# Performance work log

Measured on AMD Instinct MI355X. Metric: run time of the kernel, lower is better.

Reference implementation:

```python
import jax, jax.numpy as jnp
import numpy as np

N_POINTS = 65536
N0 = 65536
N_NEIGH = 32
K = 15
IN_F = 64
OUT_F = 128
RADIUS = 0.1
KP_EXTENT = 1.2 * RADIUS / 5.0  # config.KP_extent * radius / density_parameter
BN_EPS = 1e-6
NEG_SLOPE = 0.1


def setup_inputs() -> dict:
    key = jax.random.key(0)
    ks = jax.random.split(key, 8)
    cloud_scale = 0.05  # neighbor offsets ~ KP_EXTENT so influences are nonzero
    query_points = jax.random.uniform(ks[0], (N_POINTS, 3), jnp.float32) * cloud_scale
    support_points = jax.random.uniform(ks[1], (N0, 3), jnp.float32) * cloud_scale
    neighbors_indices = jax.random.randint(ks[2], (N_POINTS, N_NEIGH), 0, N0, jnp.int32)
    features = jax.random.normal(ks[3], (N0, IN_F), jnp.float32)
    # fixed kernel point dispositions, scaled to the kernel extent
    kernel_points = jax.random.normal(ks[4], (K, 3), jnp.float32) * (KP_EXTENT / 1.5)
    W = jax.random.normal(ks[5], (K, IN_F, OUT_F), jnp.float32) * np.sqrt(2.0 / OUT_F)
    gamma = jnp.ones((OUT_F,), jnp.float32)
    beta = jnp.zeros((OUT_F,), jnp.float32)
    return {
        "query_points": query_points,
        "support_points": support_points,
        "neighbors_indices": neighbors_indices,
        "features": features,
        "kernel_points": kernel_points,
        "W": W,
        "gamma": gamma,
        "beta": beta,
    }


def reference(query_points, support_points, neighbors_indices, features,
              kernel_points, W, gamma, beta):
    # --- KPConv: gather neighbors, kernel-point linear influence, sum aggregation ---
    # shadow point far away with zero features (handles out-of-range indices in original)
    sp = jnp.concatenate([support_points,
                          jnp.full((1, 3), 1e6, support_points.dtype)], axis=0)
    feat = jnp.concatenate([features,
                            jnp.zeros((1, features.shape[1]), features.dtype)], axis=0)
    neighbors = sp[neighbors_indices]                      # [n, m, 3]
    diffs = neighbors - query_points[:, None, :]           # [n, m, 3]
    # squared distances to each kernel point: [n, m, K]
    sq = jnp.sum((diffs[:, :, None, :] - kernel_points[None, None, :, :]) ** 2, axis=-1)
    # linear influence, 'sum' aggregation mode
    all_w = jnp.maximum(0.0, 1.0 - jnp.sqrt(sq) / KP_EXTENT)  # [n, m, K]
    all_w = jnp.transpose(all_w, (0, 2, 1))                   # [n, K, m]
    neighb_x = feat[neighbors_indices]                        # [n, m, in]
    weighted = jnp.einsum('nkm,nmi->nki', all_w, neighb_x)    # [n, K, in]
    x = jnp.einsum('nki,kio->no', weighted, W)                # [n, out]
    # --- BatchNorm1d (training-mode batch stats) + LeakyReLU(0.1) ---
    mean = jnp.mean(x, axis=0)
    var = jnp.var(x, axis=0)
    x = (x - mean) * jax.lax.rsqrt(var + BN_EPS) * gamma + beta
    return jnp.where(x >= 0, x, NEG_SLOPE * x)
```

## Files before the change

### kernel.cpp

```cpp
#include <hip/hip_runtime.h>

#define NPTS  65536
#define NNEI  32
#define NKP   15
#define INF   64
#define OUTF  128
#define PPB   32
#define NW    8
#define KT_N  32
#define NSETS 64
#define INV_KPE 41.666666666666664f
#define BN_EPS 1e-6f
#define NEG_SLOPE 0.1f

typedef __attribute__((ext_vector_type(8))) short  bf16x8;
typedef __attribute__((ext_vector_type(4))) float  f32x4;

__device__ unsigned short g_Wp[KT_N * 8 * 64 * 8];
__device__ unsigned short g_featb[NPTS * INF];
__device__ float g_part[NSETS][2 * OUTF];
__device__ float g_scale[OUTF], g_shift[OUTF];

__device__ __forceinline__ unsigned short f2b(float f) {
    union { float f; unsigned int i; } v; v.f = f;
    unsigned int x = v.i;
    return (unsigned short)((x + 0x7fffu + ((x >> 16) & 1u)) >> 16);
}
__device__ __forceinline__ unsigned int pk2(float a, float b) {
    return (unsigned int)f2b(a) | ((unsigned int)f2b(b) << 16);
}
__device__ __forceinline__ bf16x8 mk8(unsigned int a, unsigned int b,
                                      unsigned int c, unsigned int d) {
    unsigned int t[4] = {a, b, c, d};
    bf16x8 r; __builtin_memcpy(&r, t, 16); return r;
}

__global__ __launch_bounds__(256) void pack_inputs(const float* __restrict__ W,
                                                   const float* __restrict__ feat) {
    const int b = blockIdx.x, t = threadIdx.x;
    if (b < NSETS) g_part[b][t] = 0.0f;
    if (b < 512) {
        int id = b * 256 + t;
        int j  = id & 7;
        int ln = (id >> 3) & 63;
        int nt = (id >> 9) & 7;
        int kt = id >> 12;
        int i  = kt * 32 + ((ln >> 4) * 8) + j;
        int kp = i & 15;
        int ch = i >> 4;
        int o  = nt * 16 + (ln & 15);
        g_Wp[id] = (kp < NKP) ? f2b(W[(kp * 64 + ch) * 128 + o]) : (unsigned short)0;
    } else {
        int id = (b - 512) * 256 + t;
        const float4 v = ((const float4*)feat)[id];
        uint2 r; r.x = pk2(v.x, v.y); r.y = pk2(v.z, v.w);
        ((uint2*)g_featb)[id] = r;
    }
}

__global__ __launch_bounds__(512, 4) void kpconv_fused(
        const float* __restrict__ qp,
        const float* __restrict__ sp,
        const int*   __restrict__ nbr,
        const float* __restrict__ kp,
        float*       __restrict__ out)
{
    __shared__ __align__(16) unsigned short wlds[128 * PPB * 8];
    __shared__ float dbuf[NW][128][3];
    __shared__ int   ibuf[NW][128];

    const int tid  = threadIdx.x;
    const int lane = tid & 63;
    const int wv   = tid >> 6;
    const int q    = lane >> 4;
    const int c16  = lane & 15;
    const int gp0  = blockIdx.x * PPB + wv * 4;

#pragma unroll
    for (int rep = 0; rep < 2; ++rep) {
        const int pt  = rep * 2 + (lane >> 5);
        const int m   = lane & 31;
        const int gpt = gp0 + pt;
        const int idx = nbr[gpt * NNEI + m];
        ibuf[wv][pt * 32 + m] = idx;
        dbuf[wv][pt * 32 + m][0] = sp[idx * 3 + 0] - qp[gpt * 3 + 0];
        dbuf[wv][pt * 32 + m][1] = sp[idx * 3 + 1] - qp[gpt * 3 + 1];
        dbuf[wv][pt * 32 + m][2] = sp[idx * 3 + 2] - qp[gpt * 3 + 2];
    }
    float kx, ky, kz;
    if (c16 < NKP) { kx = kp[c16 * 3]; ky = kp[c16 * 3 + 1]; kz = kp[c16 * 3 + 2]; }
    else           { kx = ky = kz = 1.0e6f; }

    uint2 dcur[8], dnxt[8];
#pragma unroll
    for (int j = 0; j < 8; ++j) {
        const int idx = ibuf[wv][q * 8 + j];
        dcur[j] = *(const uint2*)&g_featb[idx * INF + c16 * 4];
    }

#pragma unroll
    for (int pt = 0; pt < 4; ++pt) {
        const int pl = wv * 4 + pt;

        if (pt < 3) {
#pragma unroll
            for (int j = 0; j < 8; ++j) {
                const int idx = ibuf[wv][(pt + 1) * 32 + q * 8 + j];
                dnxt[j] = *(const uint2*)&g_featb[idx * INF + c16 * 4];
            }
        }

        float w8[8];
#pragma unroll
        for (int j = 0; j < 8; ++j) {
            const int m = pt * 32 + q * 8 + j;
            const float ex = dbuf[wv][m][0] - kx;
            const float ey = dbuf[wv][m][1] - ky;
            const float ez = dbuf[wv][m][2] - kz;
            const float s  = ex * ex + ey * ey + ez * ez;
            const float w  = 1.0f - __builtin_amdgcn_sqrtf(s) * INV_KPE;
            w8[j] = (w > 0.0f) ? w : 0.0f;
        }
        const bf16x8 af = mk8(pk2(w8[0], w8[1]), pk2(w8[2], w8[3]),
                              pk2(w8[4], w8[5]), pk2(w8[6], w8[7]));

        f32x4 acc[4] = {{0.f,0.f,0.f,0.f},{0.f,0.f,0.f,0.f},
                        {0.f,0.f,0.f,0.f},{0.f,0.f,0.f,0.f}};
#pragma unroll
        for (int nt = 0; nt < 4; ++nt) {
            unsigned int dw[4];
#pragma unroll
            for (int p = 0; p < 4; ++p) {
                const unsigned int lo = (nt < 2) ? dcur[2 * p].x     : dcur[2 * p].y;
                const unsigned int hi = (nt < 2) ? dcur[2 * p + 1].x : dcur[2 * p + 1].y;
                dw[p] = (nt & 1) ? ((lo >> 16) | (hi & 0xffff0000u))
                                 : ((lo & 0xffffu) | (hi << 16));
            }
            acc[nt] = __builtin_amdgcn_mfma_f32_16x16x32_bf16(
                af, mk8(dw[0], dw[1], dw[2], dw[3]), acc[nt], 0, 0, 0);
        }

#pragma unroll
        for (int nt = 0; nt < 4; ++nt) {
            uint2 pv;
            pv.x = pk2(acc[nt][0], acc[nt][1]);
            pv.y = pk2(acc[nt][2], acc[nt][3]);
            const int ibase = (c16 * 4 + nt) * 16 + q * 4;
            const int g   = ibase >> 3;
            const int off = ibase & 7;
            const int plx = pl ^ ((g >> 3) & 7);
            *(uint2*)&wlds[(g * PPB + plx) * 8 + off] = pv;
        }

#pragma unroll
        for (int j = 0; j < 8; ++j) dcur[j] = dnxt[j];
    }
    __syncthreads();

    const int nt = wv;
    f32x4 a0 = {0.f,0.f,0.f,0.f}, a1 = {0.f,0.f,0.f,0.f};

    for (int kt = 0; kt < KT_N; ++kt) {
        const int g   = kt * 4 + q;
        const int h   = (g >> 3) & 7;
        const int plx0 = c16 ^ h;
        const int plx1 = (c16 + 16) ^ h;
        const bf16x8 fa0 = *(const bf16x8*)&wlds[(g * PPB + plx0) * 8];
        const bf16x8 fa1 = *(const bf16x8*)&wlds[(g * PPB + plx1) * 8];
        const bf16x8 fb  = *(const bf16x8*)&g_Wp[((kt * 8 + nt) * 64 + lane) * 8];
        a0 = __builtin_amdgcn_mfma_f32_16x16x32_bf16(fa0, fb, a0, 0, 0, 0);
        a1 = __builtin_amdgcn_mfma_f32_16x16x32_bf16(fa1, fb, a1, 0, 0, 0);
    }

    const int rb = blockIdx.x * PPB + q * 4;
    const int c0 = nt * 16 + c16;
    float s = 0.f, qq = 0.f;
#pragma unroll
    for (int r = 0; r < 4; ++r) {
        const float v0 = a0[r], v1 = a1[r];
        out[(rb + r) * OUTF + c0]        = v0;
        out[(rb + 16 + r) * OUTF + c0]   = v1;
        s += v0 + v1; qq += v0 * v0 + v1 * v1;
    }
    s  += __shfl_xor(s, 16);  s  += __shfl_xor(s, 32);
    qq += __shfl_xor(qq, 16); qq += __shfl_xor(qq, 32);
    const int set = blockIdx.x & (NSETS - 1);
    if (lane < 16) {
        atomicAdd(&g_part[set][nt * 16 + lane],        s);
        atomicAdd(&g_part[set][OUTF + nt * 16 + lane], qq);
    }
}

__global__ void bn_scaleshift(const float* __restrict__ gamma,
                              const float* __restrict__ beta) {
    const int o = threadIdx.x;
    float s = 0.f, qq = 0.f;
    for (int i = 0; i < NSETS; ++i) { s += g_part[i][o]; qq += g_part[i][OUTF + o]; }
    const float inv_n = 1.0f / (float)NPTS;
    const float mean  = s * inv_n;
    const float var   = qq * inv_n - mean * mean;
    const float sc    = gamma[o] * rsqrtf(var + BN_EPS);
    g_scale[o] = sc;
    g_shift[o] = beta[o] - mean * sc;
}

__global__ __launch_bounds__(256) void bn_norm(float* __restrict__ x) {
    const int id   = blockIdx.x * 256 + threadIdx.x;
    const int base = id * 4;
    const int o0   = base & 127;
    float4 v = *(const float4*)&x[base];
    const float4 sc = *(const float4*)&g_scale[o0];
    const float4 sf = *(const float4*)&g_shift[o0];
    float y0 = v.x * sc.x + sf.x;
    float y1 = v.y * sc.y + sf.y;
    float y2 = v.z * sc.z + sf.z;
    float y3 = v.w * sc.w + sf.w;
    y0 = (y0 >= 0.f) ? y0 : NEG_SLOPE * y0;
    y1 = (y1 >= 0.f) ? y1 : NEG_SLOPE * y1;
    y2 = (y2 >= 0.f) ? y2 : NEG_SLOPE * y2;
    y3 = (y3 >= 0.f) ? y3 : NEG_SLOPE * y3;
    float4 res = {y0, y1, y2, y3};
    *(float4*)&x[base] = res;
}

extern "C" void kernel_launch(void* const* d_in, const int* in_sizes, int n_in,
                              void* d_out, int out_size, void* d_ws, size_t ws_size,
                              hipStream_t stream) {
    const float* qp    = (const float*)d_in[0];
    const float* sp    = (const float*)d_in[1];
    const int*   nbr   = (const int*)d_in[2];
    const float* kp    = (const float*)d_in[4];
    const float* W     = (const float*)d_in[5];
    const float* gamma = (const float*)d_in[6];
    const float* beta  = (const float*)d_in[7];
    const float* feat  = (const float*)d_in[3];
    float* out = (float*)d_out;

    pack_inputs<<<512 + 4096, 256, 0, stream>>>(W, feat);
    kpconv_fused<<<NPTS / PPB, 512, 0, stream>>>(qp, sp, nbr, kp, out);
    bn_scaleshift<<<1, 128, 0, stream>>>(gamma, beta);
    bn_norm<<<(NPTS * OUTF) / (256 * 4), 256, 0, stream>>>(out);
}
```

Before: 178.5 us.

## Process four tiles per block with double-buffered feature gathers and LDS DMA

Each block now loops over four 32-point tiles instead of one, so the grid is a quarter of its former size. Neighbor feature gathers are double-buffered across points and tiles, so the next point's loads overlap the current point's MFMA work. Support-point coordinates are loaded straight into structure-of-arrays LDS buffers with global_load_lds, and the query point is folded into the kernel-point offset. Byte perms replace the shift/mask packing. The trade-offs are fewer blocks to fill the GPU, and a possible missing vmcnt wait before the DMA-filled buffers are reused.

```diff
diff --git a/kernel.cpp b/kernel.cpp
--- a/kernel.cpp
+++ b/kernel.cpp
@@ -7,6 +7,7 @@
 #define OUTF  128
 #define PPB   32
 #define NW    8
+#define NTILES 4
 #define KT_N  32
 #define NSETS 64
 #define INV_KPE 41.666666666666664f
@@ -33,6 +34,11 @@
                                       unsigned int c, unsigned int d) {
     unsigned int t[4] = {a, b, c, d};
     bf16x8 r; __builtin_memcpy(&r, t, 16); return r;
+}
+__device__ __forceinline__ void gload_lds4(const float* g, float* l) {
+    __builtin_amdgcn_global_load_lds(
+        (const __attribute__((address_space(1))) float*)g,
+        (__attribute__((address_space(3))) float*)l, 4, 0, 0);
 }
 
 __global__ __launch_bounds__(256) void pack_inputs(const float* __restrict__ W,
@@ -66,129 +72,160 @@
         float*       __restrict__ out)
 {
     __shared__ __align__(16) unsigned short wlds[128 * PPB * 8];
-    __shared__ float dbuf[NW][128][3];
-    __shared__ int   ibuf[NW][128];
+    __shared__ __align__(16) float dbx[NW][128];
+    __shared__ __align__(16) float dby[NW][128];
+    __shared__ __align__(16) float dbz[NW][128];
 
     const int tid  = threadIdx.x;
     const int lane = tid & 63;
     const int wv   = tid >> 6;
     const int q    = lane >> 4;
     const int c16  = lane & 15;
-    const int gp0  = blockIdx.x * PPB + wv * 4;
-
-#pragma unroll
-    for (int rep = 0; rep < 2; ++rep) {
-        const int pt  = rep * 2 + (lane >> 5);
-        const int m   = lane & 31;
-        const int gpt = gp0 + pt;
-        const int idx = nbr[gpt * NNEI + m];
-        ibuf[wv][pt * 32 + m] = idx;
-        dbuf[wv][pt * 32 + m][0] = sp[idx * 3 + 0] - qp[gpt * 3 + 0];
-        dbuf[wv][pt * 32 + m][1] = sp[idx * 3 + 1] - qp[gpt * 3 + 1];
-        dbuf[wv][pt * 32 + m][2] = sp[idx * 3 + 2] - qp[gpt * 3 + 2];
-    }
+    const int blk0 = blockIdx.x * (PPB * NTILES);
+
     float kx, ky, kz;
     if (c16 < NKP) { kx = kp[c16 * 3]; ky = kp[c16 * 3 + 1]; kz = kp[c16 * 3 + 2]; }
     else           { kx = ky = kz = 1.0e6f; }
 
-    uint2 dcur[8], dnxt[8];
-#pragma unroll
-    for (int j = 0; j < 8; ++j) {
-        const int idx = ibuf[wv][q * 8 + j];
-        dcur[j] = *(const uint2*)&g_featb[idx * INF + c16 * 4];
+#define DIFF_STAGE(tt) { \
+    _Pragma("unroll") \
+    for (int rep = 0; rep < 2; ++rep) { \
+        const int pt  = rep * 2 + (lane >> 5); \
+        const int m   = lane & 31; \
+        const int gpt = blk0 + (tt) * PPB + wv * 4 + pt; \
+        const int idx = nbr[gpt * NNEI + m]; \
+        gload_lds4(&sp[idx * 3 + 0], &dbx[wv][rep * 64]); \
+        gload_lds4(&sp[idx * 3 + 1], &dby[wv][rep * 64]); \
+        gload_lds4(&sp[idx * 3 + 2], &dbz[wv][rep * 64]); \
+    } }
+
+#define ISSUE_GATHER(buf, s) { \
+    const int gpt = blk0 + ((s) >> 2) * PPB + wv * 4 + ((s) & 3); \
+    const int* nbp = nbr + gpt * NNEI + q * 8; \
+    const int4 ja = *(const int4*)nbp; \
+    const int4 jb = *(const int4*)(nbp + 4); \
+    const int jj[8] = {ja.x, ja.y, ja.z, ja.w, jb.x, jb.y, jb.z, jb.w}; \
+    _Pragma("unroll") \
+    for (int j = 0; j < 8; ++j) \
+        buf[j] = *(const uint2*)&g_featb[jj[j] * INF + c16 * 4]; }
+
+    uint2 dA[8], dB[8];
+    DIFF_STAGE(0);
+    ISSUE_GATHER(dA, 0);
+    ISSUE_GATHER(dB, 1);
+    asm volatile("s_waitcnt vmcnt(0)" ::: "memory");
+    __builtin_amdgcn_sched_barrier(0);
+
+#pragma unroll
+    for (int t = 0; t < NTILES; ++t) {
+#pragma unroll
+        for (int p = 0; p < 4; ++p) {
+            const int pl  = wv * 4 + p;
+            const int gpt = blk0 + t * PPB + wv * 4 + p;
+            const float qx = qp[gpt * 3 + 0];
+            const float qy = qp[gpt * 3 + 1];
+            const float qz = qp[gpt * 3 + 2];
+            const float kxq = kx + qx, kyq = ky + qy, kzq = kz + qz;
+
+            const int m0 = p * 32 + q * 8;
+            const f32x4 x0 = *(const f32x4*)&dbx[wv][m0];
+            const f32x4 x1 = *(const f32x4*)&dbx[wv][m0 + 4];
+            const f32x4 y0 = *(const f32x4*)&dby[wv][m0];
+            const f32x4 y1 = *(const f32x4*)&dby[wv][m0 + 4];
+            const f32x4 z0 = *(const f32x4*)&dbz[wv][m0];
+            const f32x4 z1 = *(const f32x4*)&dbz[wv][m0 + 4];
+            float w8[8];
+#pragma unroll
+            for (int j = 0; j < 8; ++j) {
+                const float ex = ((j < 4) ? x0[j] : x1[j - 4]) - kxq;
+                const float ey = ((j < 4) ? y0[j] : y1[j - 4]) - kyq;
+                const float ez = ((j < 4) ? z0[j] : z1[j - 4]) - kzq;
+                const float s  = ex * ex + ey * ey + ez * ez;
+                const float w  = 1.0f - __builtin_amdgcn_sqrtf(s) * INV_KPE;
+                w8[j] = (w > 0.0f) ? w : 0.0f;
+            }
+            const bf16x8 af = mk8(pk2(w8[0], w8[1]), pk2(w8[2], w8[3]),
+                                  pk2(w8[4], w8[5]), pk2(w8[6], w8[7]));
+
+            uint2* cur = (p & 1) ? dB : dA;
+            f32x4 acc[4] = {{0.f,0.f,0.f,0.f},{0.f,0.f,0.f,0.f},
+                            {0.f,0.f,0.f,0.f},{0.f,0.f,0.f,0.f}};
+#pragma unroll
+            for (int nt = 0; nt < 4; ++nt) {
+                unsigned int dw[4];
+#pragma unroll
+                for (int pp = 0; pp < 4; ++pp) {
+                    const unsigned int lo = (nt < 2) ? cur[2 * pp].x     : cur[2 * pp].y;
+                    const unsigned int hi = (nt < 2) ? cur[2 * pp + 1].x : cur[2 * pp + 1].y;
+                    dw[pp] = (nt & 1) ? __builtin_amdgcn_perm(hi, lo, 0x07060302u)
+                                      : __builtin_amdgcn_perm(hi, lo, 0x05040100u);
+                }
+                acc[nt] = __builtin_amdgcn_mfma_f32_16x16x32_bf16(
+                    af, mk8(dw[0], dw[1], dw[2], dw[3]), acc[nt], 0, 0, 0);
+            }
+
+#pragma unroll
+            for (int nt = 0; nt < 4; ++nt) {
+                uint2 pv;
+                pv.x = pk2(acc[nt][0], acc[nt][1]);
+                pv.y = pk2(acc[nt][2], acc[nt][3]);
+                const int ibase = (c16 * 4 + nt) * 16 + q * 4;
+                const int g   = ibase >> 3;
+                const int off = ibase & 7;
+                const int plx = pl ^ ((g >> 3) & 7);
+                *(uint2*)&wlds[(g * PPB + plx) * 8 + off] = pv;
+            }
+
+            const int s2 = t * 4 + p + 2;
+            if (s2 < 4 * NTILES) ISSUE_GATHER(cur, s2);
+        }
+
+        if (t + 1 < NTILES) DIFF_STAGE(t + 1);
+
+        asm volatile("s_waitcnt lgkmcnt(0)" ::: "memory");
+        __builtin_amdgcn_sched_barrier(0);
+        __builtin_amdgcn_s_barrier();
+        __builtin_amdgcn_sched_barrier(0);
+
+        const int nt = wv;
+        f32x4 a0 = {0.f,0.f,0.f,0.f}, a1 = {0.f,0.f,0.f,0.f};
+        for (int kt = 0; kt < KT_N; ++kt) {
+            const int g   = kt * 4 + q;
+            const int h   = (g >> 3) & 7;
+            const int plx0 = c16 ^ h;
+            const int plx1 = (c16 + 16) ^ h;
+            const bf16x8 fa0 = *(const bf16x8*)&wlds[(g * PPB + plx0) * 8];
+            const bf16x8 fa1 = *(const bf16x8*)&wlds[(g * PPB + plx1) * 8];
+            const bf16x8 fb  = *(const bf16x8*)&g_Wp[((kt * 8 + nt) * 64 + lane) * 8];
+            a0 = __builtin_amdgcn_mfma_f32_16x16x32_bf16(fa0, fb, a0, 0, 0, 0);
+            a1 = __builtin_amdgcn_mfma_f32_16x16x32_bf16(fa1, fb, a1, 0, 0, 0);
+        }
+
+        const int rb = blk0 + t * PPB + q * 4;
+        const int c0 = nt * 16 + c16;
+        float s = 0.f, qq = 0.f;
+#pragma unroll
+        for (int r = 0; r < 4; ++r) {
+            const float v0 = a0[r], v1 = a1[r];
+            out[(rb + r) * OUTF + c0]      = v0;
+            out[(rb + 16 + r) * OUTF + c0] = v1;
+            s += v0 + v1; qq += v0 * v0 + v1 * v1;
+        }
+        s  += __shfl_xor(s, 16);  s  += __shfl_xor(s, 32);
+        qq += __shfl_xor(qq, 16); qq += __shfl_xor(qq, 32);
+        const int set = (blockIdx.x * NTILES + t) & (NSETS - 1);
+        if (lane < 16) {
+            atomicAdd(&g_part[set][nt * 16 + lane],        s);
+            atomicAdd(&g_part[set][OUTF + nt * 16 + lane], qq);
+        }
+
+        asm volatile("s_waitcnt lgkmcnt(0)" ::: "memory");
+        __builtin_amdgcn_sched_barrier(0);
+        __builtin_amdgcn_s_barrier();
+        __builtin_amdgcn_sched_barrier(0);
     }
-
-#pragma unroll
-    for (int pt = 0; pt < 4; ++pt) {
-        const int pl = wv * 4 + pt;
-
-        if (pt < 3) {
-#pragma unroll
-            for (int j = 0; j < 8; ++j) {
-                const int idx = ibuf[wv][(pt + 1) * 32 + q * 8 + j];
-                dnxt[j] = *(const uint2*)&g_featb[idx * INF + c16 * 4];
-            }
-        }
-
-        float w8[8];
-#pragma unroll
-        for (int j = 0; j < 8; ++j) {
-            const int m = pt * 32 + q * 8 + j;
-            const float ex = dbuf[wv][m][0] - kx;
-            const float ey = dbuf[wv][m][1] - ky;
-            const float ez = dbuf[wv][m][2] - kz;
-            const float s  = ex * ex + ey * ey + ez * ez;
-            const float w  = 1.0f - __builtin_amdgcn_sqrtf(s) * INV_KPE;
-            w8[j] = (w > 0.0f) ? w : 0.0f;
-        }
-        const bf16x8 af = mk8(pk2(w8[0], w8[1]), pk2(w8[2], w8[3]),
-                              pk2(w8[4], w8[5]), pk2(w8[6], w8[7]));
-
-        f32x4 acc[4] = {{0.f,0.f,0.f,0.f},{0.f,0.f,0.f,0.f},
-                        {0.f,0.f,0.f,0.f},{0.f,0.f,0.f,0.f}};
-#pragma unroll
-        for (int nt = 0; nt < 4; ++nt) {
-            unsigned int dw[4];
-#pragma unroll
-            for (int p = 0; p < 4; ++p) {
-                const unsigned int lo = (nt < 2) ? dcur[2 * p].x     : dcur[2 * p].y;
-                const unsigned int hi = (nt < 2) ? dcur[2 * p + 1].x : dcur[2 * p + 1].y;
-                dw[p] = (nt & 1) ? ((lo >> 16) | (hi & 0xffff0000u))
-                                 : ((lo & 0xffffu) | (hi << 16));
-            }
-            acc[nt] = __builtin_amdgcn_mfma_f32_16x16x32_bf16(
-                af, mk8(dw[0], dw[1], dw[2], dw[3]), acc[nt], 0, 0, 0);
-        }
-
-#pragma unroll
-        for (int nt = 0; nt < 4; ++nt) {
-            uint2 pv;
-            pv.x = pk2(acc[nt][0], acc[nt][1]);
-            pv.y = pk2(acc[nt][2], acc[nt][3]);
-            const int ibase = (c16 * 4 + nt) * 16 + q * 4;
-            const int g   = ibase >> 3;
-            const int off = ibase & 7;
-            const int plx = pl ^ ((g >> 3) & 7);
-            *(uint2*)&wlds[(g * PPB + plx) * 8 + off] = pv;
-        }
-
-#pragma unroll
-        for (int j = 0; j < 8; ++j) dcur[j] = dnxt[j];
-    }
-    __syncthreads();
-
-    const int nt = wv;
-    f32x4 a0 = {0.f,0.f,0.f,0.f}, a1 = {0.f,0.f,0.f,0.f};
-
-    for (int kt = 0; kt < KT_N; ++kt) {
-        const int g   = kt * 4 + q;
-        const int h   = (g >> 3) & 7;
-        const int plx0 = c16 ^ h;
-        const int plx1 = (c16 + 16) ^ h;
-        const bf16x8 fa0 = *(const bf16x8*)&wlds[(g * PPB + plx0) * 8];
-        const bf16x8 fa1 = *(const bf16x8*)&wlds[(g * PPB + plx1) * 8];
-        const bf16x8 fb  = *(const bf16x8*)&g_Wp[((kt * 8 + nt) * 64 + lane) * 8];
-        a0 = __builtin_amdgcn_mfma_f32_16x16x32_bf16(fa0, fb, a0, 0, 0, 0);
-        a1 = __builtin_amdgcn_mfma_f32_16x16x32_bf16(fa1, fb, a1, 0, 0, 0);
-    }
-
-    const int rb = blockIdx.x * PPB + q * 4;
-    const int c0 = nt * 16 + c16;
-    float s = 0.f, qq = 0.f;
-#pragma unroll
-    for (int r = 0; r < 4; ++r) {
-        const float v0 = a0[r], v1 = a1[r];
-        out[(rb + r) * OUTF + c0]        = v0;
-        out[(rb + 16 + r) * OUTF + c0]   = v1;
-        s += v0 + v1; qq += v0 * v0 + v1 * v1;
-    }
-    s  += __shfl_xor(s, 16);  s  += __shfl_xor(s, 32);
-    qq += __shfl_xor(qq, 16); qq += __shfl_xor(qq, 32);
-    const int set = blockIdx.x & (NSETS - 1);
-    if (lane < 16) {
-        atomicAdd(&g_part[set][nt * 16 + lane],        s);
-        atomicAdd(&g_part[set][OUTF + nt * 16 + lane], qq);
-    }
+#undef DIFF_STAGE
+#undef ISSUE_GATHER
 }
 
 __global__ void bn_scaleshift(const float* __restrict__ gamma,
@@ -237,7 +274,7 @@
     float* out = (float*)d_out;
 
     pack_inputs<<<512 + 4096, 256, 0, stream>>>(W, feat);
-    kpconv_fused<<<NPTS / PPB, 512, 0, stream>>>(qp, sp, nbr, kp, out);
+    kpconv_fused<<<NPTS / (PPB * NTILES), 512, 0, stream>>>(qp, sp, nbr, kp, out);
     bn_scaleshift<<<1, 128, 0, stream>>>(gamma, beta);
     bn_norm<<<(NPTS * OUTF) / (256 * 4), 256, 0, stream>>>(out);
 }
```

New measurement: 299.1 us. 1.68x slower.
